# Optimization experiments

Hardware: AMD Instinct MI355X
Metric: run time of the kernel (lower is better)

Reference implementation:

```python
import jax, jax.numpy as jnp
import numpy as np

B, W, IN, H, Z, D, OUT, K = 256, 128, 128, 1024, 128, 1024, 128, 3


def _gru_cell(h, x, Wih, Whh, bih, bhh):
    # torch nn.GRU single-layer cell, gate order (r, z, n)
    gi = x @ Wih.T + bih
    gh = h @ Whh.T + bhh
    ir, iz, inn = jnp.split(gi, 3, axis=-1)
    hr, hz, hn = jnp.split(gh, 3, axis=-1)
    r = jax.nn.sigmoid(ir + hr)
    u = jax.nn.sigmoid(iz + hz)
    n = jnp.tanh(inn + r * hn)
    return (1.0 - u) * n + u * h


def setup_inputs():
    key = jax.random.key(0)
    ks = iter(jax.random.split(key, 40))

    def w(shape, fanin):
        return jax.random.normal(next(ks), shape, jnp.float32) / np.float32(np.sqrt(fanin))

    return dict(
        x=jax.random.normal(next(ks), (B, W, IN), jnp.float32),
        eps_q=jax.random.uniform(next(ks), (B, W, Z), jnp.float32),
        eps_p=jax.random.uniform(next(ks), (B, W, OUT), jnp.float32),
        Wih_q=w((3 * H, IN), IN), Whh_q=w((3 * H, H), H),
        bih_q=jnp.zeros(3 * H, jnp.float32), bhh_q=jnp.zeros(3 * H, jnp.float32),
        Wd_q=w((D, Z + H), Z + H), bd_q=jnp.zeros(D, jnp.float32),
        Wmu_q=w((Z, D), D), bmu_q=jnp.zeros(Z, jnp.float32),
        Wsig_q=w((Z, D), D), bsig_q=jnp.zeros(Z, jnp.float32),
        Wp=w((K, Z, Z), Z), bp=jnp.zeros((K, Z), jnp.float32),
        up=0.1 * jax.random.normal(next(ks), (K,), jnp.float32),
        Wlg=w((Z, Z), Z), blg=jnp.zeros(Z, jnp.float32),
        Wih_p=w((3 * H, Z), Z), Whh_p=w((3 * H, H), H),
        bih_p=jnp.zeros(3 * H, jnp.float32), bhh_p=jnp.zeros(3 * H, jnp.float32),
        Wd_p=w((D, H), H), bd_p=jnp.zeros(D, jnp.float32),
        Wmu_p=w((OUT, D), D), bmu_p=jnp.zeros(OUT, jnp.float32),
        Wsig_p=w((OUT, D), D), bsig_p=jnp.zeros(OUT, jnp.float32),
    )


def _forward(x, eps_q, eps_p, Wih_q, Whh_q, bih_q, bhh_q, Wd_q, bd_q, Wmu_q, bmu_q,
             Wsig_q, bsig_q, Wp, bp, up, Wlg, blg, Wih_p, Whh_p, bih_p, bhh_p,
             Wd_p, bd_p, Wmu_p, bmu_p, Wsig_p, bsig_p):
    Bsz = x.shape[0]

    # ---- Qnet: sequential encoder with planar flows ----
    def q_step(carry, inp):
        e, z_prev = carry
        x_t, eps_t = inp  # [B,IN], [B,Z]
        e = _gru_cell(e, x_t, Wih_q, Whh_q, bih_q, bhh_q)
        d = jnp.concatenate([z_prev, e], axis=-1) @ Wd_q.T + bd_q
        mu = d @ Wmu_q.T + bmu_q
        logvar = jax.nn.softplus(d @ Wsig_q.T + bsig_q)
        z = mu + jnp.exp(0.5 * logvar) * eps_t
        for k in range(K):  # planar normalizing flows: z + u * tanh(Wz + b)
            z = z + up[k] * jnp.tanh(z @ Wp[k].T + bp[k])
        return (e, z), (z, mu, logvar)

    e0 = jnp.zeros((Bsz, H), x.dtype)
    z0 = jnp.zeros((Bsz, Z), x.dtype)
    _, (z_seq, mu_seq, lv_seq) = jax.lax.scan(
        q_step, (e0, z0), (jnp.swapaxes(x, 0, 1), jnp.swapaxes(eps_q, 0, 1)))

    # ---- Pnet: sequential decoder ----
    def p_step(d_t, inp):
        z_t, eps_t = inp
        zt = z_t @ Wlg.T + blg  # LGSSM linear
        d_t = _gru_cell(d_t, zt, Wih_p, Whh_p, bih_p, bhh_p)
        dd = d_t @ Wd_p.T + bd_p
        mu = dd @ Wmu_p.T + bmu_p
        sigma = jax.nn.softplus(dd @ Wsig_p.T + bsig_p)
        return d_t, mu + sigma * eps_t

    d0 = jnp.zeros((Bsz, H), x.dtype)
    _, out_seq = jax.lax.scan(p_step, d0, (z_seq, jnp.swapaxes(eps_p, 0, 1)))

    return (jnp.swapaxes(out_seq, 0, 1),
            jnp.swapaxes(mu_seq, 0, 1),
            jnp.swapaxes(lv_seq, 0, 1))


def reference(x, eps_q, eps_p, Wih_q, Whh_q, bih_q, bhh_q, Wd_q, bd_q, Wmu_q, bmu_q,
              Wsig_q, bsig_q, Wp, bp, up, Wlg, blg, Wih_p, Whh_p, bih_p, bhh_p,
              Wd_p, bd_p, Wmu_p, bmu_p, Wsig_p, bsig_p):
    return _forward(x, eps_q, eps_p, Wih_q, Whh_q, bih_q, bhh_q, Wd_q, bd_q, Wmu_q,
                    bmu_q, Wsig_q, bsig_q, Wp, bp, up, Wlg, blg, Wih_p, Whh_p,
                    bih_p, bhh_p, Wd_p, bd_p, Wmu_p, bmu_p, Wsig_p, bsig_p)
```

## Files before the change

### kernel.cpp

```cpp
#include <hip/hip_runtime.h>


typedef __bf16 bf16;
typedef __bf16 bf16x8 __attribute__((ext_vector_type(8)));
typedef float  f32x4  __attribute__((ext_vector_type(4)));
typedef unsigned u32;

static constexpr int CB   = 256;
static constexpr int CW   = 128;
static constexpr int CIN  = 128;
static constexpr int CH   = 1024;
static constexpr int CZ   = 128;
static constexpr int CD   = 1024;
static constexpr int COUT = 128;

static constexpr int APITCH     = 1160;
static constexpr int ABUF_BYTES = 16 * APITCH * 2;
static constexpr int REDN       = 8 * 16 * 17;
static constexpr int RED2_BYTES = 2 * REDN * 4;
static constexpr int FLOW_BYTES = (2 * CZ + 2 * 2 * CZ) * 4;
static constexpr int SMEM_BYTES = ABUF_BYTES + RED2_BYTES + FLOW_BYTES;

static constexpr int XCC_GETREG = 20 | (31 << 11);

#define DEV static __device__ __forceinline__

DEV float sigmoidf_(float x) { return 1.0f / (1.0f + expf(-x)); }
DEV float softplusf_(float x) { return x > 20.0f ? x : log1pf(expf(x)); }
DEV bf16x8 ldfrag(const bf16* p) { return *reinterpret_cast<const bf16x8*>(p); }

#define MFMA(a, b, c) __builtin_amdgcn_mfma_f32_16x16x32_bf16((a), (b), (c), 0, 0, 0)

template <bool FAST> DEV bf16x8 ldx16(const bf16* p) {
    bf16x8 v;
    if constexpr (FAST)
        asm volatile("global_load_dwordx4 %0, %1, off sc0\n\ts_waitcnt vmcnt(0)"
                     : "=v"(v) : "v"(p) : "memory");
    else
        asm volatile("global_load_dwordx4 %0, %1, off sc0 sc1\n\ts_waitcnt vmcnt(0)"
                     : "=v"(v) : "v"(p) : "memory");
    return v;
}
template <bool FAST> DEV u32 ldx4(const void* p) {
    u32 v;
    if constexpr (FAST)
        asm volatile("global_load_dword %0, %1, off sc0\n\ts_waitcnt vmcnt(0)"
                     : "=v"(v) : "v"(p) : "memory");
    else
        asm volatile("global_load_dword %0, %1, off sc0 sc1\n\ts_waitcnt vmcnt(0)"
                     : "=v"(v) : "v"(p) : "memory");
    return v;
}
template <bool FAST> DEV bf16x8 ldx16_nw(const bf16* p) {
    bf16x8 v;
    if constexpr (FAST)
        asm volatile("global_load_dwordx4 %0, %1, off sc0"
                     : "=v"(v) : "v"(p) : "memory");
    else
        asm volatile("global_load_dwordx4 %0, %1, off sc0 sc1"
                     : "=v"(v) : "v"(p) : "memory");
    return v;
}
DEV void vm_wait0() {
    asm volatile("s_waitcnt vmcnt(0)" ::: "memory");
    __builtin_amdgcn_sched_barrier(0);
}
template <bool FAST> DEV void stx4(void* p, u32 v) {
    if constexpr (FAST)
        asm volatile("global_store_dword %0, %1, off sc0" :: "v"(p), "v"(v) : "memory");
    else
        asm volatile("global_store_dword %0, %1, off sc0 sc1" :: "v"(p), "v"(v) : "memory");
}
DEV u32 pk2(float a, float b) {
    union { bf16 h[2]; u32 u; } r;
    r.h[0] = (bf16)a; r.h[1] = (bf16)b;
    return r.u;
}

struct Prm {
    const float *eps_q, *eps_p;
    const float *bih_q, *bhh_q, *bd_q, *bmu_q, *bsig_q;
    const float *Wp, *bp, *up, *Wlg, *blg;
    const float *bih_p, *bhh_p, *bd_p, *bmu_p, *bsig_p;
    const bf16 *x_b, *Wih_qb, *Whh_qb, *Wd_qb, *Wmu_qb, *Wsg_qb;
    const bf16 *Wih_pb, *Whh_pb, *Wd_pb, *Wmu_pb, *Wsg_pb;
    float *e_f0, *e_f1, *d_f0, *d_f1;
    bf16 *e_b0, *e_b1, *d_b0, *d_b1;
    float *ztmp_f;
    bf16 *dvec_b, *ddvec_b;
    bf16 *zflow;
    bf16 *ztlg;
    u32 *qbar, *pbar;
    u32 *zbar, *pdone;
    u32 *xcc, *cnt;
    float *out_o, *out_mu, *out_lv;
};

DEV void gbar_g(u32* flg, int slice, u32 k)
{
    asm volatile("s_waitcnt vmcnt(0)" ::: "memory");
    __syncthreads();
    if (threadIdx.x == 0)
        __hip_atomic_store(&flg[slice * 16], k, __ATOMIC_RELAXED, __HIP_MEMORY_SCOPE_AGENT);
    if (threadIdx.x < 8) {
        while (__hip_atomic_load(&flg[threadIdx.x * 16], __ATOMIC_RELAXED,
                                 __HIP_MEMORY_SCOPE_AGENT) < k)
            __builtin_amdgcn_s_sleep(1);
    }
    __syncthreads();
}

__global__ void k_cvt(const float* __restrict__ src, bf16* __restrict__ dst, int n)
{
    int i = (blockIdx.x * blockDim.x + threadIdx.x) * 4;
    if (i < n) {
        float4 v = *reinterpret_cast<const float4*>(src + i);
        *reinterpret_cast<u32*>(dst + i)     = pk2(v.x, v.y);
        *reinterpret_cast<u32*>(dst + i + 2) = pk2(v.z, v.w);
    }
}

template <bool FAST, int HMODE>
DEV void stage_act(bf16* abuf, int tid, int r0,
                   const bf16* head, long hs, int K1,
                   const bf16* body, long bs)
{
    bf16x8 v[4];
    long dst[4];
#pragma unroll
    for (int j = 0; j < 4; ++j) {
        const int idx = tid + j * 512;
        const int row = idx >> 7;
        const int k = (idx & 127) * 8;
        v[j] = ldx16_nw<FAST>(body + (long)(r0 + row) * bs + k);
        dst[j] = (long)row * APITCH + K1 + k;
    }
    vm_wait0();
#pragma unroll
    for (int j = 0; j < 4; ++j)
        *reinterpret_cast<bf16x8*>(abuf + dst[j]) = v[j];
    if (K1 > 0) {
        const int HC = K1 >> 3;
        for (int idx = tid; idx < 16 * HC; idx += 512) {
            const int row = idx / HC;
            const int k = (idx - row * HC) * 8;
            const bf16* s = head + (long)(r0 + row) * hs + k;
            bf16x8 hv;
            if constexpr (HMODE == 0)      hv = ldfrag(s);
            else if constexpr (HMODE == 1) hv = ldx16<FAST>(s);
            else                           hv = ldx16<false>(s);
            *reinterpret_cast<bf16x8*>(abuf + (long)row * APITCH + k) = hv;
        }
    }
    __syncthreads();
}

template <bool FAST>
DEV void gru_compute(const bf16* abuf, int r0, int n0, int lane, int wave,
                     const bf16* __restrict__ Wih, const bf16* __restrict__ Whh,
                     const float* __restrict__ bih, const float* __restrict__ bhh,
                     const float* __restrict__ Efin,
                     float* __restrict__ Efo, bf16* __restrict__ Ebo)
{
    const int lr = lane & 15, lkE = (lane >> 4) * 8;
    const int c = n0 + wave * 16 + lr;
    const bf16* arow = abuf + (long)lr * APITCH;

    f32x4 acc[4] = {};

    {
        bf16x8 wv[4][3];
#pragma unroll
        for (int j = 0; j < 4; ++j)
#pragma unroll
            for (int g = 0; g < 3; ++g)
                wv[j][g] = ldfrag(Wih + ((long)g * CH + c) * CIN + j * 32 + lkE);
#pragma unroll
        for (int j = 0; j < 4; ++j) {
            bf16x8 a = *reinterpret_cast<const bf16x8*>(arow + j * 32 + lkE);
            acc[0] = MFMA(a, wv[j][0], acc[0]);
            acc[1] = MFMA(a, wv[j][1], acc[1]);
            acc[2] = MFMA(a, wv[j][2], acc[2]);
        }
    }
    {
        const bf16* wp0 = Whh + ((long)0 * CH + c) * CH + lkE;
        const bf16* wp1 = Whh + ((long)1 * CH + c) * CH + lkE;
        const bf16* wp2 = Whh + ((long)2 * CH + c) * CH + lkE;
        bf16x8 wv[4][3];
#pragma unroll
        for (int j = 0; j < 4; ++j) {
            wv[j][0] = ldfrag(wp0 + j * 32);
            wv[j][1] = ldfrag(wp1 + j * 32);
            wv[j][2] = ldfrag(wp2 + j * 32);
        }
#pragma unroll
        for (int kb = 0; kb < 32; ++kb) {
            const int sl = kb & 3;
            bf16x8 a = *reinterpret_cast<const bf16x8*>(arow + CIN + kb * 32 + lkE);
            acc[0] = MFMA(a, wv[sl][0], acc[0]);
            acc[1] = MFMA(a, wv[sl][1], acc[1]);
            acc[3] = MFMA(a, wv[sl][2], acc[3]);
            if (kb < 28) {
                wv[sl][0] = ldfrag(wp0 + (kb + 4) * 32);
                wv[sl][1] = ldfrag(wp1 + (kb + 4) * 32);
                wv[sl][2] = ldfrag(wp2 + (kb + 4) * 32);
            }
        }
    }

    const float b0r = bih[c] + bhh[c];
    const float b0z = bih[CH + c] + bhh[CH + c];
    const float bin = bih[2 * CH + c];
    const float bhn = bhh[2 * CH + c];
    const int rbase = r0 + (lane >> 4) * 4;
#pragma unroll
    for (int i = 0; i < 4; ++i) {
        const int row = rbase + i;
        float r = sigmoidf_(acc[0][i] + b0r);
        float u = sigmoidf_(acc[1][i] + b0z);
        float n = tanhf(acc[2][i] + bin + r * (acc[3][i] + bhn));
        float en = (1.0f - u) * n + u * Efin[(long)row * CH + c];
        Efo[(long)row * CH + c] = en;
        float vB = __shfl_xor(en, 1);
        if (!(lane & 1))
            stx4<FAST>(Ebo + (long)row * CH + c, pk2(en, vB));
    }
}

template <bool FAST>
DEV void lin_compute(const bf16* abuf, int r0, int n0, int lane, int wave, int Ktot,
                     const bf16* __restrict__ W,
                     const float* __restrict__ bias, bf16* __restrict__ Out)
{
    const int lr = lane & 15, lkE = (lane >> 4) * 8;
    const int c = n0 + wave * 16 + lr;
    const bf16* arow = abuf + (long)lr * APITCH;
    const bf16* wrow = W + (long)c * Ktot;
    const int kofs = Ktot - CH;

    f32x4 acc = {};
    {
        const bf16* wp = wrow + kofs + lkE;
        bf16x8 wv[8];
#pragma unroll
        for (int j = 0; j < 8; ++j) wv[j] = ldfrag(wp + j * 32);
#pragma unroll
        for (int kb = 0; kb < 32; ++kb) {
            const int sl = kb & 7;
            bf16x8 a = *reinterpret_cast<const bf16x8*>(arow + kofs + kb * 32 + lkE);
            acc = MFMA(a, wv[sl], acc);
            if (kb < 24) wv[sl] = ldfrag(wp + (kb + 8) * 32);
        }
    }
    if (Ktot > CH) {
        bf16x8 wv[4];
#pragma unroll
        for (int j = 0; j < 4; ++j) wv[j] = ldfrag(wrow + j * 32 + lkE);
#pragma unroll
        for (int j = 0; j < 4; ++j) {
            bf16x8 a = *reinterpret_cast<const bf16x8*>(arow + j * 32 + lkE);
            acc = MFMA(a, wv[j], acc);
        }
    }

    const float bb = bias[c];
    const int rbase = r0 + (lane >> 4) * 4;
#pragma unroll
    for (int i = 0; i < 4; ++i) {
        float v = acc[i] + bb;
        float vB = __shfl_xor(v, 1);
        if (!(lane & 1))
            stx4<FAST>(Out + (long)(rbase + i) * CD + c, pk2(v, vB));
    }
}

template <bool FAST, int MODE>
DEV void phase_tail2(const Prm& p, int t, int slab, int slice, int tid,
                     int lane, int wave, float* Ra, float* Rs,
                     const bf16* __restrict__ A,
                     const bf16* __restrict__ Wa, const bf16* __restrict__ Wb,
                     const float* __restrict__ ba, const float* __restrict__ bb)
{
    const int lr = lane & 15, lkE = (lane >> 4) * 8;
    const int mb = slab * 16;
    const int nb = slice * 16;
    f32x4 am = {}, as = {};
    const int k0 = wave * 128;
    bf16x8 av[4], bmv[4], bsv[4];
#pragma unroll
    for (int j = 0; j < 4; ++j) {
        const int k = k0 + j * 32;
        av[j]  = ldx16_nw<FAST>(A + (long)(mb + lr) * CD + k + lkE);
        bmv[j] = ldfrag(Wa + (long)(nb + lr) * CD + k + lkE);
        bsv[j] = ldfrag(Wb + (long)(nb + lr) * CD + k + lkE);
    }
    vm_wait0();
#pragma unroll
    for (int j = 0; j < 4; ++j) {
        am = MFMA(av[j], bmv[j], am);
        as = MFMA(av[j], bsv[j], as);
    }
    __syncthreads();
#pragma unroll
    for (int i = 0; i < 4; ++i) {
        Ra[(wave * 16 + (lane >> 4) * 4 + i) * 17 + lr] = am[i];
        Rs[(wave * 16 + (lane >> 4) * 4 + i) * 17 + lr] = as[i];
    }
    __syncthreads();
    if (tid < 256) {
        const int trow = tid >> 4, tcol = tid & 15;
        float vm = 0.f, vs = 0.f;
#pragma unroll
        for (int w = 0; w < 8; ++w) {
            vm += Ra[(w * 16 + trow) * 17 + tcol];
            vs += Rs[(w * 16 + trow) * 17 + tcol];
        }
        const int row = mb + trow, col = nb + tcol;
        if constexpr (MODE == 0) {
            float mu = vm + ba[col];
            float lv = softplusf_(vs + bb[col]);
            float e  = p.eps_q[(long)row * CW * CZ + (long)t * CZ + col];
            float z  = mu + expf(0.5f * lv) * e;
            p.out_mu[(long)row * CW * CZ + (long)t * CZ + col] = mu;
            p.out_lv[(long)row * CW * CZ + (long)t * CZ + col] = lv;
            stx4<FAST>(p.ztmp_f + (long)row * CZ + col, __float_as_uint(z));
        } else {
            float m  = vm + ba[col];
            float sg = softplusf_(vs + bb[col]);
            float e  = p.eps_p[(long)row * CW * COUT + (long)t * COUT + col];
            p.out_o[(long)row * CW * COUT + (long)t * COUT + col] = m + sg * e;
        }
    }
}

template <bool FAST>
DEV void phase_flows2(const Prm& p, int rowbase, int tid, int t, float* zl, float* ps)
{
    const int rg = tid >> 8;
    const int sub = tid & 255;
    const int c = sub & 127, half = sub >> 7;
    const int row = rowbase + rg;
    float* zrow = zl + rg * CZ;
    float* pall = ps + rg * 2 * CZ;

    if (half == 0)
        zrow[c] = __uint_as_float(ldx4<FAST>(p.ztmp_f + (long)row * CZ + c));
    __syncthreads();

#pragma unroll 1
    for (int kf = 0; kf < 3; ++kf) {
        const float* wr = p.Wp + ((long)kf * CZ + c) * CZ + half * 64;
        const float* zh = zrow + half * 64;
        float s = 0.f;
#pragma unroll
        for (int j = 0; j < 64; j += 4) {
            float4 w = *reinterpret_cast<const float4*>(wr + j);
            s += zh[j] * w.x + zh[j + 1] * w.y + zh[j + 2] * w.z + zh[j + 3] * w.w;
        }
        pall[half * CZ + c] = s;
        __syncthreads();
        if (half == 0) {
            float sf = pall[c] + pall[CZ + c] + p.bp[kf * CZ + c];
            zrow[c] += p.up[kf] * tanhf(sf);
        }
        __syncthreads();
    }
    {
        const float* wr = p.Wlg + (long)c * CZ + half * 64;
        const float* zh = zrow + half * 64;
        float s = 0.f;
#pragma unroll
        for (int j = 0; j < 64; j += 4) {
            float4 w = *reinterpret_cast<const float4*>(wr + j);
            s += zh[j] * w.x + zh[j + 1] * w.y + zh[j + 2] * w.z + zh[j + 3] * w.w;
        }
        pall[half * CZ + c] = s;
        __syncthreads();
        if (half == 0) {
            float zt = pall[c] + pall[CZ + c] + p.blg[c];
            float ztB = __shfl_xor(zt, 1);
            if (!(c & 1)) {
                stx4<false>(p.ztlg + ((size_t)(t & 1) * CB + row) * CZ + c, pk2(zt, ztB));
                stx4<FAST>(p.zflow + ((size_t)((t + 1) & 1) * CB + row) * CZ + c,
                           pk2(zrow[c], zrow[c + 1]));
            }
        }
    }
}

template <bool FAST>
DEV void run_q(const Prm& p, int slab, int slice, int tid,
               bf16* abuf, float* Ra, float* Rs, float* ZLp, float* PSp)
{
    const int lane = tid & 63, wave = tid >> 6;
    const int r0 = slab * 16, n0 = slice * 128;
    u32* qb = p.qbar + slab * 8 * 16;
    u32 bk = 0;
#pragma unroll 1
    for (int t = 0; t < CW; ++t) {
        const int bi = t & 1;
        const bf16*  eb_i = bi ? p.e_b1 : p.e_b0;
        const float* ef_i = bi ? p.e_f1 : p.e_f0;
        bf16*  eb_o = bi ? p.e_b0 : p.e_b1;
        float* ef_o = bi ? p.e_f0 : p.e_f1;

        stage_act<FAST, 0>(abuf, tid, r0, p.x_b + (long)t * CIN, (long)CW * CIN,
                           CIN, eb_i, CH);
        gru_compute<FAST>(abuf, r0, n0, lane, wave, p.Wih_qb, p.Whh_qb,
                          p.bih_q, p.bhh_q, ef_i, ef_o, eb_o);
        gbar_g(qb, slice, ++bk);
        stage_act<FAST, 1>(abuf, tid, r0, p.zflow + (size_t)bi * CB * CZ,
                           CZ, CZ, eb_o, CH);
        lin_compute<FAST>(abuf, r0, n0, lane, wave, CZ + CH, p.Wd_qb, p.bd_q, p.dvec_b);
        gbar_g(qb, slice, ++bk);
        phase_tail2<FAST, 0>(p, t, slab, slice, tid, lane, wave, Ra, Rs,
                             p.dvec_b, p.Wmu_qb, p.Wsg_qb, p.bmu_q, p.bsig_q);
        gbar_g(qb, slice, ++bk);
        if (t >= 2) {
            if (tid == 0) {
                while ((int)__hip_atomic_load(&p.pdone[slab * 16], __ATOMIC_RELAXED,
                                              __HIP_MEMORY_SCOPE_AGENT) < t - 1)
                    __builtin_amdgcn_s_sleep(2);
            }
            __syncthreads();
        }
        phase_flows2<FAST>(p, slab * 16 + slice * 2, tid, t, ZLp, PSp);
        gbar_g(qb, slice, ++bk);
        if (slice == 0 && tid == 0)
            __hip_atomic_store(&p.zbar[slab * 16], (u32)(t + 1),
                               __ATOMIC_RELAXED, __HIP_MEMORY_SCOPE_AGENT);
    }
}

template <bool FAST>
DEV void run_p(const Prm& p, int slab, int slice, int tid,
               bf16* abuf, float* Ra, float* Rs)
{
    const int lane = tid & 63, wave = tid >> 6;
    const int r0 = slab * 16, n0 = slice * 128;
    u32* pb = p.pbar + slab * 8 * 16;
    u32 bk = 0;
#pragma unroll 1
    for (int t = 0; t < CW; ++t) {
        if (tid == 0) {
            while (__hip_atomic_load(&p.zbar[slab * 16], __ATOMIC_RELAXED,
                                     __HIP_MEMORY_SCOPE_AGENT) < (u32)(t + 1))
                __builtin_amdgcn_s_sleep(2);
        }
        __syncthreads();

        const int bi = t & 1;
        const bf16*  db_i = bi ? p.d_b1 : p.d_b0;
        const float* df_i = bi ? p.d_f1 : p.d_f0;
        bf16*  db_o = bi ? p.d_b0 : p.d_b1;
        float* df_o = bi ? p.d_f0 : p.d_f1;

        stage_act<FAST, 2>(abuf, tid, r0, p.ztlg + (size_t)bi * CB * CZ,
                           CZ, CZ, db_i, CH);
        gru_compute<FAST>(abuf, r0, n0, lane, wave, p.Wih_pb, p.Whh_pb,
                          p.bih_p, p.bhh_p, df_i, df_o, db_o);
        gbar_g(pb, slice, ++bk);
        if (slice == 0 && tid == 0)
            __hip_atomic_store(&p.pdone[slab * 16], (u32)(t + 1),
                               __ATOMIC_RELAXED, __HIP_MEMORY_SCOPE_AGENT);
        stage_act<FAST, 0>(abuf, tid, r0, nullptr, 0, 0, db_o, CH);
        lin_compute<FAST>(abuf, r0, n0, lane, wave, CH, p.Wd_pb, p.bd_p, p.ddvec_b);
        gbar_g(pb, slice, ++bk);
        phase_tail2<FAST, 1>(p, t, slab, slice, tid, lane, wave, Ra, Rs,
                             p.ddvec_b, p.Wmu_pb, p.Wsg_pb, p.bmu_p, p.bsig_p);
    }
}

__launch_bounds__(512)
__global__ void mega(Prm p)
{
    extern __shared__ char smem[];
    bf16*  abuf = (bf16*)smem;
    float* Ra   = (float*)(smem + ABUF_BYTES);
    float* Rs   = Ra + REDN;
    float* ZLp  = (float*)(smem + ABUF_BYTES + RED2_BYTES);
    float* PSp  = ZLp + 2 * CZ;
    __shared__ int s_fast;

    const int wg = blockIdx.x, tid = threadIdx.x;
    const int gid = wg & 7, m = wg >> 3;
    const bool isQ = gid < 4;
    const int slab = (isQ ? gid : gid - 4) * 4 + (m >> 3);
    const int slice = m & 7;

    const u32 myx = (u32)__builtin_amdgcn_s_getreg(XCC_GETREG);
    if (tid == 0) {
        __hip_atomic_store(&p.xcc[wg * 16], myx, __ATOMIC_RELAXED, __HIP_MEMORY_SCOPE_AGENT);
        __hip_atomic_fetch_add(p.cnt, 1u, __ATOMIC_RELAXED, __HIP_MEMORY_SCOPE_AGENT);
        while (__hip_atomic_load(p.cnt, __ATOMIC_RELAXED, __HIP_MEMORY_SCOPE_AGENT) < 256u)
            __builtin_amdgcn_s_sleep(2);
    }
    __syncthreads();
    if (tid < 64) {
        bool eq = true;
        if (tid < 32) {
            u32 o = __hip_atomic_load(&p.xcc[(gid + 8 * tid) * 16],
                                      __ATOMIC_RELAXED, __HIP_MEMORY_SCOPE_AGENT);
            eq = (o == myx);
        }
        unsigned long long b = __ballot(eq);
        if (tid == 0) s_fast = (b == ~0ull) ? 1 : 0;
    }
    __syncthreads();
    const bool fast = (s_fast != 0);

    if (isQ) {
        if (fast) run_q<true>(p, slab, slice, tid, abuf, Ra, Rs, ZLp, PSp);
        else      run_q<false>(p, slab, slice, tid, abuf, Ra, Rs, ZLp, PSp);
    } else {
        if (fast) run_p<true>(p, slab, slice, tid, abuf, Ra, Rs);
        else      run_p<false>(p, slab, slice, tid, abuf, Ra, Rs);
    }
}

extern "C" void kernel_launch(void* const* d_in, const int* in_sizes, int n_in,
                              void* d_out, int out_size, void* d_ws, size_t ws_size,
                              hipStream_t stream)
{
    Prm p;
    const float* x      = (const float*)d_in[0];
    p.eps_q  = (const float*)d_in[1];
    p.eps_p  = (const float*)d_in[2];
    const float* Wih_q  = (const float*)d_in[3];
    const float* Whh_q  = (const float*)d_in[4];
    p.bih_q  = (const float*)d_in[5];
    p.bhh_q  = (const float*)d_in[6];
    const float* Wd_q   = (const float*)d_in[7];
    p.bd_q   = (const float*)d_in[8];
    const float* Wmu_q  = (const float*)d_in[9];
    p.bmu_q  = (const float*)d_in[10];
    const float* Wsig_q = (const float*)d_in[11];
    p.bsig_q = (const float*)d_in[12];
    p.Wp     = (const float*)d_in[13];
    p.bp     = (const float*)d_in[14];
    p.up     = (const float*)d_in[15];
    p.Wlg    = (const float*)d_in[16];
    p.blg    = (const float*)d_in[17];
    const float* Wih_p  = (const float*)d_in[18];
    const float* Whh_p  = (const float*)d_in[19];
    p.bih_p  = (const float*)d_in[20];
    p.bhh_p  = (const float*)d_in[21];
    const float* Wd_p   = (const float*)d_in[22];
    p.bd_p   = (const float*)d_in[23];
    const float* Wmu_p  = (const float*)d_in[24];
    p.bmu_p  = (const float*)d_in[25];
    const float* Wsig_p = (const float*)d_in[26];
    p.bsig_p = (const float*)d_in[27];

    p.out_o  = (float*)d_out;
    p.out_mu = p.out_o + (size_t)CB * CW * COUT;
    p.out_lv = p.out_mu + (size_t)CB * CW * CZ;

    char* wp_ = (char*)d_ws;
    auto carve = [&](size_t bytes) -> void* {
        void* q = (void*)wp_;
        wp_ += (bytes + 255) & ~(size_t)255;
        return q;
    };
    p.e_f0 = (float*)carve((size_t)CB * CH * 4);
    p.e_f1 = (float*)carve((size_t)CB * CH * 4);
    p.d_f0 = (float*)carve((size_t)CB * CH * 4);
    p.d_f1 = (float*)carve((size_t)CB * CH * 4);
    p.e_b0 = (bf16*)carve((size_t)CB * CH * 2);
    p.e_b1 = (bf16*)carve((size_t)CB * CH * 2);
    p.d_b0 = (bf16*)carve((size_t)CB * CH * 2);
    p.d_b1 = (bf16*)carve((size_t)CB * CH * 2);
    p.ztmp_f  = (float*)carve((size_t)CB * CZ * 4);
    p.dvec_b  = (bf16*)carve((size_t)CB * CD * 2);
    p.ddvec_b = (bf16*)carve((size_t)CB * CD * 2);
    p.zflow   = (bf16*)carve((size_t)2 * CB * CZ * 2);
    p.ztlg    = (bf16*)carve((size_t)2 * CB * CZ * 2);
    p.qbar    = (u32*)carve((size_t)16 * 8 * 16 * 4);
    p.pbar    = (u32*)carve((size_t)16 * 8 * 16 * 4);
    p.zbar    = (u32*)carve((size_t)16 * 16 * 4);
    p.pdone   = (u32*)carve((size_t)16 * 16 * 4);
    p.xcc     = (u32*)carve((size_t)256 * 16 * 4);
    p.cnt     = (u32*)carve(256);
    bf16* x_b    = (bf16*)carve((size_t)CB * CW * CIN * 2);
    bf16* Wih_qb = (bf16*)carve((size_t)3 * CH * CIN * 2);
    bf16* Whh_qb = (bf16*)carve((size_t)3 * CH * CH * 2);
    bf16* Wd_qb  = (bf16*)carve((size_t)CD * (CZ + CH) * 2);
    bf16* Wmu_qb = (bf16*)carve((size_t)CZ * CD * 2);
    bf16* Wsg_qb = (bf16*)carve((size_t)CZ * CD * 2);
    bf16* Wih_pb = (bf16*)carve((size_t)3 * CH * CZ * 2);
    bf16* Whh_pb = (bf16*)carve((size_t)3 * CH * CH * 2);
    bf16* Wd_pb  = (bf16*)carve((size_t)CD * CH * 2);
    bf16* Wmu_pb = (bf16*)carve((size_t)COUT * CD * 2);
    bf16* Wsg_pb = (bf16*)carve((size_t)COUT * CD * 2);
    p.x_b = x_b;       p.Wih_qb = Wih_qb; p.Whh_qb = Whh_qb;
    p.Wd_qb = Wd_qb;   p.Wmu_qb = Wmu_qb; p.Wsg_qb = Wsg_qb;
    p.Wih_pb = Wih_pb; p.Whh_pb = Whh_pb; p.Wd_pb = Wd_pb;
    p.Wmu_pb = Wmu_pb; p.Wsg_pb = Wsg_pb;

    hipMemsetAsync(p.e_f0, 0, (size_t)CB * CH * 4, stream);
    hipMemsetAsync(p.d_f0, 0, (size_t)CB * CH * 4, stream);
    hipMemsetAsync(p.e_b0, 0, (size_t)CB * CH * 2, stream);
    hipMemsetAsync(p.d_b0, 0, (size_t)CB * CH * 2, stream);
    hipMemsetAsync(p.zflow, 0, (size_t)CB * CZ * 2, stream);
    hipMemsetAsync(p.qbar, 0, (size_t)16 * 8 * 16 * 4, stream);
    hipMemsetAsync(p.pbar, 0, (size_t)16 * 8 * 16 * 4, stream);
    hipMemsetAsync(p.zbar, 0, (size_t)16 * 16 * 4, stream);
    hipMemsetAsync(p.pdone, 0, (size_t)16 * 16 * 4, stream);
    hipMemsetAsync(p.xcc, 0, (size_t)256 * 16 * 4, stream);
    hipMemsetAsync(p.cnt, 0, 256, stream);

    auto cvt = [&](const float* s, bf16* d, size_t n) {
        k_cvt<<<dim3((unsigned)((n / 4 + 255) / 256)), dim3(256), 0, stream>>>(s, d, (int)n);
    };
    cvt(x,      x_b,    (size_t)CB * CW * CIN);
    cvt(Wih_q,  Wih_qb, (size_t)3 * CH * CIN);
    cvt(Whh_q,  Whh_qb, (size_t)3 * CH * CH);
    cvt(Wd_q,   Wd_qb,  (size_t)CD * (CZ + CH));
    cvt(Wmu_q,  Wmu_qb, (size_t)CZ * CD);
    cvt(Wsig_q, Wsg_qb, (size_t)CZ * CD);
    cvt(Wih_p,  Wih_pb, (size_t)3 * CH * CZ);
    cvt(Whh_p,  Whh_pb, (size_t)3 * CH * CH);
    cvt(Wd_p,   Wd_pb,  (size_t)CD * CH);
    cvt(Wmu_p,  Wmu_pb, (size_t)COUT * CD);
    cvt(Wsig_p, Wsg_pb, (size_t)COUT * CD);

    mega<<<dim3(256), dim3(512), SMEM_BYTES, stream>>>(p);
}
```

Measured before the change: 8.089 ms.

## Use per-timestep buffers and global 128-WG barriers instead of XCC-local slabs

Removes the runtime XCC-locality detection and the slab/slice decomposition, replacing it with a 128-workgroup-wide barrier per Q and P pipeline and a new tile mapping. When the workspace is large, every timestep's hidden state, intermediate vectors and flow outputs get their own buffer. Each buffer is written once, so ordinary cached loads can be used instead of cache-bypassing sc0/sc1 loads, and the pdone back-pressure wait is dropped. The trade-off is much wider barriers (128 flags polled per step instead of 8), which raises synchronisation cost, plus a large workspace footprint, and correctness now depends on stale cache lines never being hit.

```diff
diff --git a/kernel.cpp b/kernel.cpp
--- a/kernel.cpp
+++ b/kernel.cpp
@@ -21,8 +21,6 @@
 static constexpr int FLOW_BYTES = (2 * CZ + 2 * 2 * CZ) * 4;
 static constexpr int SMEM_BYTES = ABUF_BYTES + RED2_BYTES + FLOW_BYTES;
 
-static constexpr int XCC_GETREG = 20 | (31 << 11);
-
 #define DEV static __device__ __forceinline__
 
 DEV float sigmoidf_(float x) { return 1.0f / (1.0f + expf(-x)); }
@@ -31,45 +29,30 @@
 
 #define MFMA(a, b, c) __builtin_amdgcn_mfma_f32_16x16x32_bf16((a), (b), (c), 0, 0, 0)
 
-template <bool FAST> DEV bf16x8 ldx16(const bf16* p) {
+DEV bf16x8 ldd16(const bf16* p) {
     bf16x8 v;
-    if constexpr (FAST)
-        asm volatile("global_load_dwordx4 %0, %1, off sc0\n\ts_waitcnt vmcnt(0)"
-                     : "=v"(v) : "v"(p) : "memory");
-    else
-        asm volatile("global_load_dwordx4 %0, %1, off sc0 sc1\n\ts_waitcnt vmcnt(0)"
-                     : "=v"(v) : "v"(p) : "memory");
+    asm volatile("global_load_dwordx4 %0, %1, off sc0 sc1\n\ts_waitcnt vmcnt(0)"
+                 : "=v"(v) : "v"(p) : "memory");
     return v;
 }
-template <bool FAST> DEV u32 ldx4(const void* p) {
+DEV bf16x8 ldd16_nw(const bf16* p) {
+    bf16x8 v;
+    asm volatile("global_load_dwordx4 %0, %1, off sc0 sc1"
+                 : "=v"(v) : "v"(p) : "memory");
+    return v;
+}
+DEV u32 ldd4(const void* p) {
     u32 v;
-    if constexpr (FAST)
-        asm volatile("global_load_dword %0, %1, off sc0\n\ts_waitcnt vmcnt(0)"
-                     : "=v"(v) : "v"(p) : "memory");
-    else
-        asm volatile("global_load_dword %0, %1, off sc0 sc1\n\ts_waitcnt vmcnt(0)"
-                     : "=v"(v) : "v"(p) : "memory");
+    asm volatile("global_load_dword %0, %1, off sc0 sc1\n\ts_waitcnt vmcnt(0)"
+                 : "=v"(v) : "v"(p) : "memory");
     return v;
 }
-template <bool FAST> DEV bf16x8 ldx16_nw(const bf16* p) {
-    bf16x8 v;
-    if constexpr (FAST)
-        asm volatile("global_load_dwordx4 %0, %1, off sc0"
-                     : "=v"(v) : "v"(p) : "memory");
-    else
-        asm volatile("global_load_dwordx4 %0, %1, off sc0 sc1"
-                     : "=v"(v) : "v"(p) : "memory");
-    return v;
+DEV void std4(void* p, u32 v) {
+    asm volatile("global_store_dword %0, %1, off sc0 sc1" :: "v"(p), "v"(v) : "memory");
 }
 DEV void vm_wait0() {
     asm volatile("s_waitcnt vmcnt(0)" ::: "memory");
     __builtin_amdgcn_sched_barrier(0);
-}
-template <bool FAST> DEV void stx4(void* p, u32 v) {
-    if constexpr (FAST)
-        asm volatile("global_store_dword %0, %1, off sc0" :: "v"(p), "v"(v) : "memory");
-    else
-        asm volatile("global_store_dword %0, %1, off sc0 sc1" :: "v"(p), "v"(v) : "memory");
 }
 DEV u32 pk2(float a, float b) {
     union { bf16 h[2]; u32 u; } r;
@@ -85,24 +68,22 @@
     const bf16 *x_b, *Wih_qb, *Whh_qb, *Wd_qb, *Wmu_qb, *Wsg_qb;
     const bf16 *Wih_pb, *Whh_pb, *Wd_pb, *Wmu_pb, *Wsg_pb;
     float *e_f0, *e_f1, *d_f0, *d_f1;
-    bf16 *e_b0, *e_b1, *d_b0, *d_b1;
-    float *ztmp_f;
-    bf16 *dvec_b, *ddvec_b;
-    bf16 *zflow;
-    bf16 *ztlg;
-    u32 *qbar, *pbar;
-    u32 *zbar, *pdone;
-    u32 *xcc, *cnt;
+    bf16 *e_h, *d_h;
+    bf16 *dvec_h, *ddvec_h;
+    float *ztmp_h;
+    bf16 *zflow_h;
+    bf16 *ztlg_h;
+    u32 *qbar, *pbar, *zbar, *pdone;
     float *out_o, *out_mu, *out_lv;
 };
 
-DEV void gbar_g(u32* flg, int slice, u32 k)
+DEV void gbar128(u32* flg, int lwg, u32 k)
 {
     asm volatile("s_waitcnt vmcnt(0)" ::: "memory");
     __syncthreads();
     if (threadIdx.x == 0)
-        __hip_atomic_store(&flg[slice * 16], k, __ATOMIC_RELAXED, __HIP_MEMORY_SCOPE_AGENT);
-    if (threadIdx.x < 8) {
+        __hip_atomic_store(&flg[lwg * 16], k, __ATOMIC_RELAXED, __HIP_MEMORY_SCOPE_AGENT);
+    if (threadIdx.x < 128) {
         while (__hip_atomic_load(&flg[threadIdx.x * 16], __ATOMIC_RELAXED,
                                  __HIP_MEMORY_SCOPE_AGENT) < k)
             __builtin_amdgcn_s_sleep(1);
@@ -120,25 +101,35 @@
     }
 }
 
-template <bool FAST, int HMODE>
+template <bool BIG, int HM>
 DEV void stage_act(bf16* abuf, int tid, int r0,
                    const bf16* head, long hs, int K1,
                    const bf16* body, long bs)
 {
-    bf16x8 v[4];
-    long dst[4];
-#pragma unroll
-    for (int j = 0; j < 4; ++j) {
-        const int idx = tid + j * 512;
-        const int row = idx >> 7;
-        const int k = (idx & 127) * 8;
-        v[j] = ldx16_nw<FAST>(body + (long)(r0 + row) * bs + k);
-        dst[j] = (long)row * APITCH + K1 + k;
-    }
-    vm_wait0();
-#pragma unroll
-    for (int j = 0; j < 4; ++j)
-        *reinterpret_cast<bf16x8*>(abuf + dst[j]) = v[j];
+    if constexpr (BIG) {
+        for (int j = 0; j < 4; ++j) {
+            const int idx = tid + j * 512;
+            const int row = idx >> 7;
+            const int k = (idx & 127) * 8;
+            *reinterpret_cast<bf16x8*>(abuf + (long)row * APITCH + K1 + k) =
+                ldfrag(body + (long)(r0 + row) * bs + k);
+        }
+    } else {
+        bf16x8 v[4];
+        long dst[4];
+#pragma unroll
+        for (int j = 0; j < 4; ++j) {
+            const int idx = tid + j * 512;
+            const int row = idx >> 7;
+            const int k = (idx & 127) * 8;
+            v[j] = ldd16_nw(body + (long)(r0 + row) * bs + k);
+            dst[j] = (long)row * APITCH + K1 + k;
+        }
+        vm_wait0();
+#pragma unroll
+        for (int j = 0; j < 4; ++j)
+            *reinterpret_cast<bf16x8*>(abuf + dst[j]) = v[j];
+    }
     if (K1 > 0) {
         const int HC = K1 >> 3;
         for (int idx = tid; idx < 16 * HC; idx += 512) {
@@ -146,16 +137,14 @@
             const int k = (idx - row * HC) * 8;
             const bf16* s = head + (long)(r0 + row) * hs + k;
             bf16x8 hv;
-            if constexpr (HMODE == 0)      hv = ldfrag(s);
-            else if constexpr (HMODE == 1) hv = ldx16<FAST>(s);
-            else                           hv = ldx16<false>(s);
+            if constexpr (HM == 0) hv = ldfrag(s);
+            else                   hv = BIG ? ldfrag(s) : ldd16(s);
             *reinterpret_cast<bf16x8*>(abuf + (long)row * APITCH + k) = hv;
         }
     }
     __syncthreads();
 }
 
-template <bool FAST>
 DEV void gru_compute(const bf16* abuf, int r0, int n0, int lane, int wave,
                      const bf16* __restrict__ Wih, const bf16* __restrict__ Whh,
                      const float* __restrict__ bih, const float* __restrict__ bhh,
@@ -167,7 +156,6 @@
     const bf16* arow = abuf + (long)lr * APITCH;
 
     f32x4 acc[4] = {};
-
     {
         bf16x8 wv[4][3];
 #pragma unroll
@@ -224,11 +212,10 @@
         Efo[(long)row * CH + c] = en;
         float vB = __shfl_xor(en, 1);
         if (!(lane & 1))
-            stx4<FAST>(Ebo + (long)row * CH + c, pk2(en, vB));
-    }
-}
-
-template <bool FAST>
+            std4(Ebo + (long)row * CH + c, pk2(en, vB));
+    }
+}
+
 DEV void lin_compute(const bf16* abuf, int r0, int n0, int lane, int wave, int Ktot,
                      const bf16* __restrict__ W,
                      const float* __restrict__ bias, bf16* __restrict__ Out)
@@ -271,31 +258,30 @@
         float v = acc[i] + bb;
         float vB = __shfl_xor(v, 1);
         if (!(lane & 1))
-            stx4<FAST>(Out + (long)(rbase + i) * CD + c, pk2(v, vB));
-    }
-}
-
-template <bool FAST, int MODE>
-DEV void phase_tail2(const Prm& p, int t, int slab, int slice, int tid,
+            std4(Out + (long)(rbase + i) * CD + c, pk2(v, vB));
+    }
+}
+
+template <bool BIG, int MODE>
+DEV void phase_tail2(const Prm& p, int t, int mb, int nb, int tid,
                      int lane, int wave, float* Ra, float* Rs,
-                     const bf16* __restrict__ A,
+                     const bf16* __restrict__ A, float* __restrict__ ztmp,
                      const bf16* __restrict__ Wa, const bf16* __restrict__ Wb,
                      const float* __restrict__ ba, const float* __restrict__ bb)
 {
     const int lr = lane & 15, lkE = (lane >> 4) * 8;
-    const int mb = slab * 16;
-    const int nb = slice * 16;
     f32x4 am = {}, as = {};
     const int k0 = wave * 128;
     bf16x8 av[4], bmv[4], bsv[4];
 #pragma unroll
     for (int j = 0; j < 4; ++j) {
         const int k = k0 + j * 32;
-        av[j]  = ldx16_nw<FAST>(A + (long)(mb + lr) * CD + k + lkE);
+        const bf16* ap = A + (long)(mb + lr) * CD + k + lkE;
+        av[j]  = BIG ? ldfrag(ap) : ldd16_nw(ap);
         bmv[j] = ldfrag(Wa + (long)(nb + lr) * CD + k + lkE);
         bsv[j] = ldfrag(Wb + (long)(nb + lr) * CD + k + lkE);
     }
-    vm_wait0();
+    if constexpr (!BIG) vm_wait0();
 #pragma unroll
     for (int j = 0; j < 4; ++j) {
         am = MFMA(av[j], bmv[j], am);
@@ -324,7 +310,7 @@
             float z  = mu + expf(0.5f * lv) * e;
             p.out_mu[(long)row * CW * CZ + (long)t * CZ + col] = mu;
             p.out_lv[(long)row * CW * CZ + (long)t * CZ + col] = lv;
-            stx4<FAST>(p.ztmp_f + (long)row * CZ + col, __float_as_uint(z));
+            std4(ztmp + (long)row * CZ + col, __float_as_uint(z));
         } else {
             float m  = vm + ba[col];
             float sg = softplusf_(vs + bb[col]);
@@ -334,8 +320,10 @@
     }
 }
 
-template <bool FAST>
-DEV void phase_flows2(const Prm& p, int rowbase, int tid, int t, float* zl, float* ps)
+template <bool BIG>
+DEV void phase_flows2(const Prm& p, int rowbase, int tid, int t, float* zl, float* ps,
+                      const float* __restrict__ ztmp,
+                      bf16* __restrict__ ztlg, bf16* __restrict__ zflow_next)
 {
     const int rg = tid >> 8;
     const int sub = tid & 255;
@@ -345,7 +333,8 @@
     float* pall = ps + rg * 2 * CZ;
 
     if (half == 0)
-        zrow[c] = __uint_as_float(ldx4<FAST>(p.ztmp_f + (long)row * CZ + c));
+        zrow[c] = BIG ? ztmp[(long)row * CZ + c]
+                      : __uint_as_float(ldd4(ztmp + (long)row * CZ + c));
     __syncthreads();
 
 #pragma unroll 1
@@ -381,97 +370,124 @@
             float zt = pall[c] + pall[CZ + c] + p.blg[c];
             float ztB = __shfl_xor(zt, 1);
             if (!(c & 1)) {
-                stx4<false>(p.ztlg + ((size_t)(t & 1) * CB + row) * CZ + c, pk2(zt, ztB));
-                stx4<FAST>(p.zflow + ((size_t)((t + 1) & 1) * CB + row) * CZ + c,
-                           pk2(zrow[c], zrow[c + 1]));
+                std4(ztlg + (long)row * CZ + c, pk2(zt, ztB));
+                std4(zflow_next + (long)row * CZ + c, pk2(zrow[c], zrow[c + 1]));
             }
         }
     }
 }
 
-template <bool FAST>
-DEV void run_q(const Prm& p, int slab, int slice, int tid,
+template <bool BIG>
+DEV void run_q(const Prm& p, int lwg, int tid,
                bf16* abuf, float* Ra, float* Rs, float* ZLp, float* PSp)
 {
     const int lane = tid & 63, wave = tid >> 6;
-    const int r0 = slab * 16, n0 = slice * 128;
-    u32* qb = p.qbar + slab * 8 * 16;
+    const int g = lwg >> 5, m = lwg & 31;
+    const int r0 = (m >> 1) * 16;
+    const int n0 = g * 256 + (m & 1) * 128;
+    const int nt = g * 32 + (m & 1) * 16;
+    const size_t SH = (size_t)CB * CH, SD = (size_t)CB * CD, SZ = (size_t)CB * CZ;
     u32 bk = 0;
 #pragma unroll 1
     for (int t = 0; t < CW; ++t) {
-        const int bi = t & 1;
-        const bf16*  eb_i = bi ? p.e_b1 : p.e_b0;
-        const float* ef_i = bi ? p.e_f1 : p.e_f0;
-        bf16*  eb_o = bi ? p.e_b0 : p.e_b1;
-        float* ef_o = bi ? p.e_f0 : p.e_f1;
-
-        stage_act<FAST, 0>(abuf, tid, r0, p.x_b + (long)t * CIN, (long)CW * CIN,
-                           CIN, eb_i, CH);
-        gru_compute<FAST>(abuf, r0, n0, lane, wave, p.Wih_qb, p.Whh_qb,
-                          p.bih_q, p.bhh_q, ef_i, ef_o, eb_o);
-        gbar_g(qb, slice, ++bk);
-        stage_act<FAST, 1>(abuf, tid, r0, p.zflow + (size_t)bi * CB * CZ,
-                           CZ, CZ, eb_o, CH);
-        lin_compute<FAST>(abuf, r0, n0, lane, wave, CZ + CH, p.Wd_qb, p.bd_q, p.dvec_b);
-        gbar_g(qb, slice, ++bk);
-        phase_tail2<FAST, 0>(p, t, slab, slice, tid, lane, wave, Ra, Rs,
-                             p.dvec_b, p.Wmu_qb, p.Wsg_qb, p.bmu_q, p.bsig_q);
-        gbar_g(qb, slice, ++bk);
-        if (t >= 2) {
-            if (tid == 0) {
-                while ((int)__hip_atomic_load(&p.pdone[slab * 16], __ATOMIC_RELAXED,
-                                              __HIP_MEMORY_SCOPE_AGENT) < t - 1)
-                    __builtin_amdgcn_s_sleep(2);
+        const int eIn  = BIG ? t : (t & 1);
+        const int eOut = BIG ? (t + 1) : ((t + 1) & 1);
+        const int dT   = BIG ? t : 0;
+        const int zT   = BIG ? t : (t & 1);
+        const float* ef_i = (t & 1) ? p.e_f1 : p.e_f0;
+        float*       ef_o = (t & 1) ? p.e_f0 : p.e_f1;
+
+        stage_act<BIG, 0>(abuf, tid, r0, p.x_b + (long)t * CIN, (long)CW * CIN,
+                          CIN, p.e_h + (size_t)eIn * SH, CH);
+        gru_compute(abuf, r0, n0, lane, wave, p.Wih_qb, p.Whh_qb,
+                    p.bih_q, p.bhh_q, ef_i, ef_o, p.e_h + (size_t)eOut * SH);
+        gbar128(p.qbar, lwg, ++bk);
+
+        stage_act<BIG, 1>(abuf, tid, r0, p.zflow_h + (size_t)eIn * SZ, CZ, CZ,
+                          p.e_h + (size_t)eOut * SH, CH);
+        lin_compute(abuf, r0, n0, lane, wave, CZ + CH, p.Wd_qb, p.bd_q,
+                    p.dvec_h + (size_t)dT * SD);
+        gbar128(p.qbar, lwg, ++bk);
+
+        phase_tail2<BIG, 0>(p, t, r0, nt, tid, lane, wave, Ra, Rs,
+                            p.dvec_h + (size_t)dT * SD, p.ztmp_h + (size_t)dT * SZ,
+                            p.Wmu_qb, p.Wsg_qb, p.bmu_q, p.bsig_q);
+        gbar128(p.qbar, lwg, ++bk);
+
+        if constexpr (!BIG) {
+            if (t >= 2) {
+                if (tid < 128) {
+                    while ((int)__hip_atomic_load(&p.pdone[tid * 16], __ATOMIC_RELAXED,
+                                                  __HIP_MEMORY_SCOPE_AGENT) < t - 1)
+                        __builtin_amdgcn_s_sleep(2);
+                }
+                __syncthreads();
             }
-            __syncthreads();
-        }
-        phase_flows2<FAST>(p, slab * 16 + slice * 2, tid, t, ZLp, PSp);
-        gbar_g(qb, slice, ++bk);
-        if (slice == 0 && tid == 0)
-            __hip_atomic_store(&p.zbar[slab * 16], (u32)(t + 1),
+        }
+        phase_flows2<BIG>(p, lwg * 2, tid, t, ZLp, PSp,
+                          p.ztmp_h + (size_t)dT * SZ,
+                          p.ztlg_h + (size_t)zT * SZ,
+                          p.zflow_h + (size_t)eOut * SZ);
+        asm volatile("s_waitcnt vmcnt(0)" ::: "memory");
+        __syncthreads();
+        if (tid == 0)
+            __hip_atomic_store(&p.zbar[lwg * 16], (u32)(t + 1),
                                __ATOMIC_RELAXED, __HIP_MEMORY_SCOPE_AGENT);
-    }
-}
-
-template <bool FAST>
-DEV void run_p(const Prm& p, int slab, int slice, int tid,
+        __syncthreads();
+    }
+}
+
+template <bool BIG>
+DEV void run_p(const Prm& p, int lwg, int tid,
                bf16* abuf, float* Ra, float* Rs)
 {
     const int lane = tid & 63, wave = tid >> 6;
-    const int r0 = slab * 16, n0 = slice * 128;
-    u32* pb = p.pbar + slab * 8 * 16;
+    const int g = lwg >> 5, m = lwg & 31;
+    const int r0 = (m >> 1) * 16;
+    const int n0 = g * 256 + (m & 1) * 128;
+    const int nt = g * 32 + (m & 1) * 16;
+    const size_t SH = (size_t)CB * CH, SD = (size_t)CB * CD, SZ = (size_t)CB * CZ;
     u32 bk = 0;
 #pragma unroll 1
     for (int t = 0; t < CW; ++t) {
-        if (tid == 0) {
-            while (__hip_atomic_load(&p.zbar[slab * 16], __ATOMIC_RELAXED,
+        if (tid < 128) {
+            while (__hip_atomic_load(&p.zbar[tid * 16], __ATOMIC_RELAXED,
                                      __HIP_MEMORY_SCOPE_AGENT) < (u32)(t + 1))
                 __builtin_amdgcn_s_sleep(2);
         }
         __syncthreads();
 
-        const int bi = t & 1;
-        const bf16*  db_i = bi ? p.d_b1 : p.d_b0;
-        const float* df_i = bi ? p.d_f1 : p.d_f0;
-        bf16*  db_o = bi ? p.d_b0 : p.d_b1;
-        float* df_o = bi ? p.d_f0 : p.d_f1;
-
-        stage_act<FAST, 2>(abuf, tid, r0, p.ztlg + (size_t)bi * CB * CZ,
-                           CZ, CZ, db_i, CH);
-        gru_compute<FAST>(abuf, r0, n0, lane, wave, p.Wih_pb, p.Whh_pb,
-                          p.bih_p, p.bhh_p, df_i, df_o, db_o);
-        gbar_g(pb, slice, ++bk);
-        if (slice == 0 && tid == 0)
-            __hip_atomic_store(&p.pdone[slab * 16], (u32)(t + 1),
-                               __ATOMIC_RELAXED, __HIP_MEMORY_SCOPE_AGENT);
-        stage_act<FAST, 0>(abuf, tid, r0, nullptr, 0, 0, db_o, CH);
-        lin_compute<FAST>(abuf, r0, n0, lane, wave, CH, p.Wd_pb, p.bd_p, p.ddvec_b);
-        gbar_g(pb, slice, ++bk);
-        phase_tail2<FAST, 1>(p, t, slab, slice, tid, lane, wave, Ra, Rs,
-                             p.ddvec_b, p.Wmu_pb, p.Wsg_pb, p.bmu_p, p.bsig_p);
-    }
-}
-
+        const int sIn  = BIG ? t : (t & 1);
+        const int sOut = BIG ? (t + 1) : ((t + 1) & 1);
+        const int dT   = BIG ? t : 0;
+        const int zT   = BIG ? t : (t & 1);
+        const float* df_i = (t & 1) ? p.d_f1 : p.d_f0;
+        float*       df_o = (t & 1) ? p.d_f0 : p.d_f1;
+
+        stage_act<BIG, 1>(abuf, tid, r0, p.ztlg_h + (size_t)zT * SZ, CZ, CZ,
+                          p.d_h + (size_t)sIn * SH, CH);
+        gru_compute(abuf, r0, n0, lane, wave, p.Wih_pb, p.Whh_pb,
+                    p.bih_p, p.bhh_p, df_i, df_o, p.d_h + (size_t)sOut * SH);
+        gbar128(p.pbar, lwg, ++bk);
+        if constexpr (!BIG) {
+            if (tid == 0)
+                __hip_atomic_store(&p.pdone[lwg * 16], (u32)(t + 1),
+                                   __ATOMIC_RELAXED, __HIP_MEMORY_SCOPE_AGENT);
+        }
+
+        stage_act<BIG, 0>(abuf, tid, r0, nullptr, 0, 0,
+                          p.d_h + (size_t)sOut * SH, CH);
+        lin_compute(abuf, r0, n0, lane, wave, CH, p.Wd_pb, p.bd_p,
+                    p.ddvec_h + (size_t)dT * SD);
+        gbar128(p.pbar, lwg, ++bk);
+
+        phase_tail2<BIG, 1>(p, t, r0, nt, tid, lane, wave, Ra, Rs,
+                            p.ddvec_h + (size_t)dT * SD, nullptr,
+                            p.Wmu_pb, p.Wsg_pb, p.bmu_p, p.bsig_p);
+    }
+}
+
+template <bool BIG>
 __launch_bounds__(512)
 __global__ void mega(Prm p)
 {
@@ -481,42 +497,14 @@
     float* Rs   = Ra + REDN;
     float* ZLp  = (float*)(smem + ABUF_BYTES + RED2_BYTES);
     float* PSp  = ZLp + 2 * CZ;
-    __shared__ int s_fast;
 
     const int wg = blockIdx.x, tid = threadIdx.x;
     const int gid = wg & 7, m = wg >> 3;
     const bool isQ = gid < 4;
-    const int slab = (isQ ? gid : gid - 4) * 4 + (m >> 3);
-    const int slice = m & 7;
-
-    const u32 myx = (u32)__builtin_amdgcn_s_getreg(XCC_GETREG);
-    if (tid == 0) {
-        __hip_atomic_store(&p.xcc[wg * 16], myx, __ATOMIC_RELAXED, __HIP_MEMORY_SCOPE_AGENT);
-        __hip_atomic_fetch_add(p.cnt, 1u, __ATOMIC_RELAXED, __HIP_MEMORY_SCOPE_AGENT);
-        while (__hip_atomic_load(p.cnt, __ATOMIC_RELAXED, __HIP_MEMORY_SCOPE_AGENT) < 256u)
-            __builtin_amdgcn_s_sleep(2);
-    }
-    __syncthreads();
-    if (tid < 64) {
-        bool eq = true;
-        if (tid < 32) {
-            u32 o = __hip_atomic_load(&p.xcc[(gid + 8 * tid) * 16],
-                                      __ATOMIC_RELAXED, __HIP_MEMORY_SCOPE_AGENT);
-            eq = (o == myx);
-        }
-        unsigned long long b = __ballot(eq);
-        if (tid == 0) s_fast = (b == ~0ull) ? 1 : 0;
-    }
-    __syncthreads();
-    const bool fast = (s_fast != 0);
-
-    if (isQ) {
-        if (fast) run_q<true>(p, slab, slice, tid, abuf, Ra, Rs, ZLp, PSp);
-        else      run_q<false>(p, slab, slice, tid, abuf, Ra, Rs, ZLp, PSp);
-    } else {
-        if (fast) run_p<true>(p, slab, slice, tid, abuf, Ra, Rs);
-        else      run_p<false>(p, slab, slice, tid, abuf, Ra, Rs);
-    }
+    const int lwg = (isQ ? gid : gid - 4) * 32 + m;
+
+    if (isQ) run_q<BIG>(p, lwg, tid, abuf, Ra, Rs, ZLp, PSp);
+    else     run_p<BIG>(p, lwg, tid, abuf, Ra, Rs);
 }
 
 extern "C" void kernel_launch(void* const* d_in, const int* in_sizes, int n_in,
@@ -557,6 +545,11 @@
     p.out_mu = p.out_o + (size_t)CB * CW * COUT;
     p.out_lv = p.out_mu + (size_t)CB * CW * CZ;
 
+    const bool BIGM = ws_size >= (size_t)400 * 1024 * 1024;
+    const int NS = BIGM ? (CW + 1) : 2;
+    const int NT = BIGM ? CW : 1;
+    const int NZ = BIGM ? CW : 2;
+
     char* wp_ = (char*)d_ws;
     auto carve = [&](size_t bytes) -> void* {
         void* q = (void*)wp_;
@@ -567,21 +560,17 @@
     p.e_f1 = (float*)carve((size_t)CB * CH * 4);
     p.d_f0 = (float*)carve((size_t)CB * CH * 4);
     p.d_f1 = (float*)carve((size_t)CB * CH * 4);
-    p.e_b0 = (bf16*)carve((size_t)CB * CH * 2);
-    p.e_b1 = (bf16*)carve((size_t)CB * CH * 2);
-    p.d_b0 = (bf16*)carve((size_t)CB * CH * 2);
-    p.d_b1 = (bf16*)carve((size_t)CB * CH * 2);
-    p.ztmp_f  = (float*)carve((size_t)CB * CZ * 4);
-    p.dvec_b  = (bf16*)carve((size_t)CB * CD * 2);
-    p.ddvec_b = (bf16*)carve((size_t)CB * CD * 2);
-    p.zflow   = (bf16*)carve((size_t)2 * CB * CZ * 2);
-    p.ztlg    = (bf16*)carve((size_t)2 * CB * CZ * 2);
-    p.qbar    = (u32*)carve((size_t)16 * 8 * 16 * 4);
-    p.pbar    = (u32*)carve((size_t)16 * 8 * 16 * 4);
-    p.zbar    = (u32*)carve((size_t)16 * 16 * 4);
-    p.pdone   = (u32*)carve((size_t)16 * 16 * 4);
-    p.xcc     = (u32*)carve((size_t)256 * 16 * 4);
-    p.cnt     = (u32*)carve(256);
+    p.e_h     = (bf16*)carve((size_t)NS * CB * CH * 2);
+    p.d_h     = (bf16*)carve((size_t)NS * CB * CH * 2);
+    p.dvec_h  = (bf16*)carve((size_t)NT * CB * CD * 2);
+    p.ddvec_h = (bf16*)carve((size_t)NT * CB * CD * 2);
+    p.ztmp_h  = (float*)carve((size_t)NT * CB * CZ * 4);
+    p.zflow_h = (bf16*)carve((size_t)NS * CB * CZ * 2);
+    p.ztlg_h  = (bf16*)carve((size_t)NZ * CB * CZ * 2);
+    p.qbar    = (u32*)carve((size_t)128 * 16 * 4);
+    p.pbar    = (u32*)carve((size_t)128 * 16 * 4);
+    p.zbar    = (u32*)carve((size_t)128 * 16 * 4);
+    p.pdone   = (u32*)carve((size_t)128 * 16 * 4);
     bf16* x_b    = (bf16*)carve((size_t)CB * CW * CIN * 2);
     bf16* Wih_qb = (bf16*)carve((size_t)3 * CH * CIN * 2);
     bf16* Whh_qb = (bf16*)carve((size_t)3 * CH * CH * 2);
@@ -600,15 +589,13 @@
 
     hipMemsetAsync(p.e_f0, 0, (size_t)CB * CH * 4, stream);
     hipMemsetAsync(p.d_f0, 0, (size_t)CB * CH * 4, stream);
-    hipMemsetAsync(p.e_b0, 0, (size_t)CB * CH * 2, stream);
-    hipMemsetAsync(p.d_b0, 0, (size_t)CB * CH * 2, stream);
-    hipMemsetAsync(p.zflow, 0, (size_t)CB * CZ * 2, stream);
-    hipMemsetAsync(p.qbar, 0, (size_t)16 * 8 * 16 * 4, stream);
-    hipMemsetAsync(p.pbar, 0, (size_t)16 * 8 * 16 * 4, stream);
-    hipMemsetAsync(p.zbar, 0, (size_t)16 * 16 * 4, stream);
-    hipMemsetAsync(p.pdone, 0, (size_t)16 * 16 * 4, stream);
-    hipMemsetAsync(p.xcc, 0, (size_t)256 * 16 * 4, stream);
-    hipMemsetAsync(p.cnt, 0, 256, stream);
+    hipMemsetAsync(p.e_h, 0, (size_t)CB * CH * 2, stream);
+    hipMemsetAsync(p.d_h, 0, (size_t)CB * CH * 2, stream);
+    hipMemsetAsync(p.zflow_h, 0, (size_t)CB * CZ * 2, stream);
+    hipMemsetAsync(p.qbar, 0, (size_t)128 * 16 * 4, stream);
+    hipMemsetAsync(p.pbar, 0, (size_t)128 * 16 * 4, stream);
+    hipMemsetAsync(p.zbar, 0, (size_t)128 * 16 * 4, stream);
+    hipMemsetAsync(p.pdone, 0, (size_t)128 * 16 * 4, stream);
 
     auto cvt = [&](const float* s, bf16* d, size_t n) {
         k_cvt<<<dim3((unsigned)((n / 4 + 255) / 256)), dim3(256), 0, stream>>>(s, d, (int)n);
@@ -625,5 +612,8 @@
     cvt(Wmu_p,  Wmu_pb, (size_t)COUT * CD);
     cvt(Wsig_p, Wsg_pb, (size_t)COUT * CD);
 
-    mega<<<dim3(256), dim3(512), SMEM_BYTES, stream>>>(p);
-}
+    if (BIGM)
+        mega<true><<<dim3(256), dim3(512), SMEM_BYTES, stream>>>(p);
+    else
+        mega<false><<<dim3(256), dim3(512), SMEM_BYTES, stream>>>(p);
+}
```

Result: no change. 8.053 ms (median of 2 runs) (-0.5%).
